# Performance work log

Hardware: AMD Instinct MI355X
Metric: run time of the kernel (lower is better)

The kernel has to match this reference:

```python
import jax, jax.numpy as jnp
import numpy as np

N = 50000      # nodes
E = 800000     # edges (avg degree 16)
F_IN = 128     # input_dim
HID = 64       # hidden_dim
HEADS = 4      # heads on first layer only
G = 512        # number of graphs in batch
EPS = 1e-5
NEG_SLOPE = 0.2

# (in_dim, out_dim, heads) per GATv2 layer
LAYER_DIMS = [(F_IN, HID, HEADS), (HID * HEADS, HID, 1), (HID, HID, 1)]


def setup_inputs() -> dict:
    key = jax.random.key(0)
    ks = jax.random.split(key, 16)
    def rn(k, shape, fan_in):
        return jax.random.normal(k, shape, jnp.float32) / np.float32(np.sqrt(fan_in))
    inp = {}
    inp["x"] = jax.random.normal(ks[0], (N, F_IN), jnp.float32)
    inp["edge_index"] = jax.random.randint(ks[1], (2, E), 0, N)
    inp["batch"] = jnp.sort(jax.random.randint(ks[2], (N,), 0, G))
    i = 3
    for l, (din, dout, h) in enumerate(LAYER_DIMS):
        kk = jax.random.split(ks[i], 3)
        inp[f"Wl{l}"] = rn(kk[0], (din, h * dout), din)
        inp[f"bl{l}"] = jnp.zeros((h * dout,), jnp.float32)
        inp[f"Wr{l}"] = rn(kk[1], (din, h * dout), din)
        inp[f"br{l}"] = jnp.zeros((h * dout,), jnp.float32)
        inp[f"att{l}"] = rn(kk[2], (h, dout), dout)
        inp[f"bias{l}"] = jnp.zeros((h * dout,), jnp.float32)
        inp[f"ln_g{l}"] = jnp.ones((h * dout,), jnp.float32)
        inp[f"ln_b{l}"] = jnp.zeros((h * dout,), jnp.float32)
        i += 1
    inp["Wh1"] = rn(ks[i], (HID, HID), HID)
    inp["bh1"] = jnp.zeros((HID,), jnp.float32)
    inp["Wh2"] = rn(ks[i + 1], (HID, 1), HID)
    inp["bh2"] = jnp.zeros((1,), jnp.float32)
    return inp


def gatv2_layer(x, src, dst, Wl, bl, Wr, br, att, bias, heads, out_c):
    """PyG GATv2Conv (concat=True, share_weights=False, eval mode)."""
    n = x.shape[0]
    xl = (x @ Wl + bl).reshape(n, heads, out_c)   # messages (source side)
    xr = (x @ Wr + br).reshape(n, heads, out_c)   # destination side
    e = jax.nn.leaky_relu(xl[src] + xr[dst], NEG_SLOPE)          # [E,H,C]
    logit = jnp.einsum('ehc,hc->eh', e, att)                      # [E,H]
    m = jax.ops.segment_max(logit, dst, num_segments=n)           # segment-softmax
    ex = jnp.exp(logit - m[dst])
    den = jax.ops.segment_sum(ex, dst, num_segments=n)
    alpha = ex / den[dst]                                         # [E,H]
    out = jax.ops.segment_sum(alpha[:, :, None] * xl[src], dst, num_segments=n)
    return out.reshape(n, heads * out_c) + bias


def graph_layernorm(h, g, b):
    """PyG LayerNorm(mode='graph') with batch=None: normalize over all elements."""
    mu = h.mean()
    xc = h - mu
    var = (xc * xc).mean()
    return xc * jax.lax.rsqrt(var + EPS) * g + b


def reference(x, edge_index, batch,
              Wl0, bl0, Wr0, br0, att0, bias0, ln_g0, ln_b0,
              Wl1, bl1, Wr1, br1, att1, bias1, ln_g1, ln_b1,
              Wl2, bl2, Wr2, br2, att2, bias2, ln_g2, ln_b2,
              Wh1, bh1, Wh2, bh2):
    src, dst = edge_index[0], edge_index[1]
    layers = [
        (Wl0, bl0, Wr0, br0, att0, bias0, ln_g0, ln_b0),
        (Wl1, bl1, Wr1, br1, att1, bias1, ln_g1, ln_b1),
        (Wl2, bl2, Wr2, br2, att2, bias2, ln_g2, ln_b2),
    ]
    h = x
    for (Wl, bl, Wr, br, att, bias, g, b), (_, dout, heads) in zip(layers, LAYER_DIMS):
        h_in = h
        h = gatv2_layer(h, src, dst, Wl, bl, Wr, br, att, bias, heads, dout)
        h = graph_layernorm(h, g, b)
        h = jax.nn.relu(h)
        if h_in.shape[1] == h.shape[1]:   # residual only when widths match
            h = h + h_in
        # dropout: identity in eval mode
    # global mean pool over graphs
    counts = jax.ops.segment_sum(jnp.ones((h.shape[0], 1), h.dtype), batch, num_segments=G)
    Z = jax.ops.segment_sum(h, batch, num_segments=G) / jnp.maximum(counts, 1.0)
    logits = jax.nn.relu(Z @ Wh1 + bh1) @ Wh2 + bh2
    return logits
```

## Files before the change

kernel.cpp:

```cpp
#include <hip/hip_runtime.h>
#include <math.h>

#define NN 50000
#define NE 800000
#define NG 512
#define LRELU 0.2f
#define LN_EPS 1e-5
#define GCAP 128
#define NBUCK 256

typedef __attribute__((ext_vector_type(8))) short short8;
typedef __attribute__((ext_vector_type(4))) float f32x4;

__global__ void hist_kernel(const int* __restrict__ dst, int* __restrict__ deg) {
    int e = blockIdx.x * blockDim.x + threadIdx.x;
    if (e < NE) atomicAdd(&deg[dst[e]], 1);
}

__global__ __launch_bounds__(1024) void scan1(const int* __restrict__ deg,
                                              int* __restrict__ excl,
                                              int* __restrict__ bsum, int n) {
    __shared__ int s[1024];
    int tid = threadIdx.x;
    int gid = blockIdx.x * 1024 + tid;
    int v = (gid < n) ? deg[gid] : 0;
    s[tid] = v;
    __syncthreads();
    for (int off = 1; off < 1024; off <<= 1) {
        int t = (tid >= off) ? s[tid - off] : 0;
        __syncthreads();
        s[tid] += t;
        __syncthreads();
    }
    if (gid < n) excl[gid] = s[tid] - v;
    if (tid == 1023) bsum[blockIdx.x] = s[1023];
}

__global__ __launch_bounds__(64) void scan2(int* __restrict__ bsum, int nb) {
    int lane = threadIdx.x;
    int v = (lane < nb) ? bsum[lane] : 0;
    int orig = v;
    #pragma unroll
    for (int off = 1; off < 64; off <<= 1) {
        int t = __shfl_up(v, off, 64);
        if (lane >= off) v += t;
    }
    if (lane < nb) bsum[lane] = v - orig;
}

__global__ __launch_bounds__(1024) void scan3(int* __restrict__ row_ptr,
                                              int* __restrict__ cursor,
                                              const int* __restrict__ bsum, int n) {
    int tid = threadIdx.x;
    int gid = blockIdx.x * 1024 + tid;
    if (gid < n) {
        int v = row_ptr[gid] + bsum[blockIdx.x];
        row_ptr[gid] = v;
        cursor[gid] = v;
    }
    if (gid == 0) row_ptr[n] = NE;
}

__global__ void scatter_kernel(const int* __restrict__ src, const int* __restrict__ dst,
                               int* __restrict__ cursor, int* __restrict__ col_src) {
    int e = blockIdx.x * blockDim.x + threadIdx.x;
    if (e < NE) {
        int pos = atomicAdd(&cursor[dst[e]], 1);
        col_src[pos] = src[e];
    }
}

__device__ inline void split_bf16(float v, ushort& h, ushort& l) {
    unsigned ub = __float_as_uint(v);
    unsigned hh = (ub + 0x7FFFu + ((ub >> 16) & 1u)) >> 16;
    float vh = __uint_as_float(hh << 16);
    float r = v - vh;
    unsigned ur = __float_as_uint(r);
    unsigned ll = (ur + 0x7FFFu + ((ur >> 16) & 1u)) >> 16;
    h = (ushort)hh; l = (ushort)ll;
}

__global__ __launch_bounds__(256) void prep_w(const float* __restrict__ Wl0,
                                              const float* __restrict__ Wr0,
                                              const float* __restrict__ Wl1,
                                              const float* __restrict__ Wr1,
                                              const float* __restrict__ Wl2,
                                              const float* __restrict__ Wr2,
                                              ushort* __restrict__ wt) {
    int id = blockIdx.x * 256 + threadIdx.x;
    const float* W; int K, N, rel; ushort* hi;
    if (id < 65536) {
        W = (id < 32768) ? Wl0 : Wr0;
        rel = id & 32767; K = 128; N = 256;
        hi = wt + ((id < 32768) ? 0 : 65536);
    } else if (id < 98304) {
        int t = id - 65536;
        W = (t < 16384) ? Wl1 : Wr1;
        rel = t & 16383; K = 256; N = 64;
        hi = wt + 131072 + ((t < 16384) ? 0 : 32768);
    } else if (id < 106496) {
        int t = id - 98304;
        W = (t < 4096) ? Wl2 : Wr2;
        rel = t & 4095; K = 64; N = 64;
        hi = wt + 196608 + ((t < 4096) ? 0 : 8192);
    } else return;
    ushort* lo = hi + K * N;
    int n = rel / K, k = rel - n * K;
    ushort h, l;
    split_bf16(W[k * N + n], h, l);
    hi[rel] = h;
    lo[rel] = l;
}

__global__ __launch_bounds__(256) void gemm_mfma(const float* __restrict__ A,
                                                 const ushort* __restrict__ Bh0,
                                                 const ushort* __restrict__ Bl0,
                                                 const float* __restrict__ bias0,
                                                 float* __restrict__ C0,
                                                 const ushort* __restrict__ Bh1,
                                                 const ushort* __restrict__ Bl1,
                                                 const float* __restrict__ bias1,
                                                 float* __restrict__ C1,
                                                 int M, int Ncol, int K,
                                                 const float* __restrict__ lnstats,
                                                 const float* __restrict__ lng,
                                                 const float* __restrict__ lnb) {
    __shared__ ushort sAh[64][40];
    __shared__ ushort sAl[64][40];
    __shared__ ushort sBh[64][40];
    __shared__ ushort sBl[64][40];
    const ushort* Bhi = blockIdx.z ? Bh1 : Bh0;
    const ushort* Blo = blockIdx.z ? Bl1 : Bl0;
    const float*  bias = blockIdx.z ? bias1 : bias0;
    float*        C = blockIdx.z ? C1 : C0;
    const int tid = threadIdx.x;
    const int row0 = blockIdx.x * 64;
    const int col0 = blockIdx.y * 64;
    const int w = tid >> 6, lane = tid & 63;
    const int fm = lane & 15;
    const int fk = (lane >> 4) * 8;
    const bool doln = (lnstats != nullptr);
    float mu = 0.f, rstd = 0.f;
    if (doln) { mu = lnstats[0]; rstd = lnstats[1]; }
    f32x4 acc[4] = {};

    for (int k0 = 0; k0 < K; k0 += 32) {
        __syncthreads();
        int f = tid;
        #pragma unroll
        for (int it = 0; it < 2; it++, f += 256) {
            int r = f >> 3, kc = (f & 7) * 4;
            int grow = row0 + r;
            float4 v = (grow < M) ? *(const float4*)&A[(size_t)grow * K + k0 + kc]
                                  : make_float4(0.f, 0.f, 0.f, 0.f);
            if (doln) {
                int c0 = k0 + kc;
                v.x = fmaxf((v.x - mu) * rstd * lng[c0 + 0] + lnb[c0 + 0], 0.f);
                v.y = fmaxf((v.y - mu) * rstd * lng[c0 + 1] + lnb[c0 + 1], 0.f);
                v.z = fmaxf((v.z - mu) * rstd * lng[c0 + 2] + lnb[c0 + 2], 0.f);
                v.w = fmaxf((v.w - mu) * rstd * lng[c0 + 3] + lnb[c0 + 3], 0.f);
            }
            ushort4 h, l;
            split_bf16(v.x, h.x, l.x);
            split_bf16(v.y, h.y, l.y);
            split_bf16(v.z, h.z, l.z);
            split_bf16(v.w, h.w, l.w);
            *(ushort4*)&sAh[r][kc] = h;
            *(ushort4*)&sAl[r][kc] = l;
        }
        int u = tid;
        #pragma unroll
        for (int it = 0; it < 2; it++, u += 256) {
            int n = u >> 3, kc = (u & 7) * 4;
            *(ushort4*)&sBh[n][kc] = *(const ushort4*)&Bhi[(size_t)(col0 + n) * K + k0 + kc];
            *(ushort4*)&sBl[n][kc] = *(const ushort4*)&Blo[(size_t)(col0 + n) * K + k0 + kc];
        }
        __syncthreads();
        short8 ah = *(const short8*)&sAh[w * 16 + fm][fk];
        short8 al = *(const short8*)&sAl[w * 16 + fm][fk];
        #pragma unroll
        for (int c = 0; c < 4; c++) {
            short8 bh = *(const short8*)&sBh[c * 16 + fm][fk];
            short8 bl = *(const short8*)&sBl[c * 16 + fm][fk];
            acc[c] = __builtin_amdgcn_mfma_f32_16x16x32_bf16(ah, bh, acc[c], 0, 0, 0);
            acc[c] = __builtin_amdgcn_mfma_f32_16x16x32_bf16(al, bh, acc[c], 0, 0, 0);
            acc[c] = __builtin_amdgcn_mfma_f32_16x16x32_bf16(ah, bl, acc[c], 0, 0, 0);
        }
    }
    const int orow = w * 16 + (lane >> 4) * 4;
    #pragma unroll
    for (int c = 0; c < 4; c++) {
        int col = col0 + c * 16 + fm;
        float bv = bias[col];
        #pragma unroll
        for (int r = 0; r < 4; r++) {
            int grow = row0 + orow + r;
            if (grow < M) C[(size_t)grow * Ncol + col] = acc[c][r] + bv;
        }
    }
}

__device__ inline float dpp_red_add16(float x) {
    x += __int_as_float(__builtin_amdgcn_update_dpp(0, __float_as_int(x), 0xB1, 0xF, 0xF, true));
    x += __int_as_float(__builtin_amdgcn_update_dpp(0, __float_as_int(x), 0x4E, 0xF, 0xF, true));
    x += __int_as_float(__builtin_amdgcn_update_dpp(0, __float_as_int(x), 0x141, 0xF, 0xF, true));
    x += __int_as_float(__builtin_amdgcn_update_dpp(0, __float_as_int(x), 0x140, 0xF, 0xF, true));
    return x;
}

__device__ inline void gat_upd_fast(const float4& xv, const float4& rxr, const float4& ratt,
                                    float& m, float& sum, float4& acc) {
    float vx = xv.x + rxr.x; vx = fmaxf(vx, vx * LRELU);
    float vy = xv.y + rxr.y; vy = fmaxf(vy, vy * LRELU);
    float vz = xv.z + rxr.z; vz = fmaxf(vz, vz * LRELU);
    float vw = xv.w + rxr.w; vw = fmaxf(vw, vw * LRELU);
    float p = vx * ratt.x;
    p = fmaf(vy, ratt.y, p);
    p = fmaf(vz, ratt.z, p);
    p = fmaf(vw, ratt.w, p);
    p = dpp_red_add16(p);
    if (__all(p <= m)) {
        float e = __expf(p - m);
        sum += e;
        acc.x = fmaf(e, xv.x, acc.x);
        acc.y = fmaf(e, xv.y, acc.y);
        acc.z = fmaf(e, xv.z, acc.z);
        acc.w = fmaf(e, xv.w, acc.w);
    } else {
        float mn = fmaxf(m, p);
        float sc = __expf(m - mn);
        float e  = __expf(p - mn);
        sum = fmaf(sum, sc, e);
        acc.x = fmaf(acc.x, sc, e * xv.x);
        acc.y = fmaf(acc.y, sc, e * xv.y);
        acc.z = fmaf(acc.z, sc, e * xv.z);
        acc.w = fmaf(acc.w, sc, e * xv.w);
        m = mn;
    }
}

__global__ __launch_bounds__(256) void gat4(const float* __restrict__ xl,
                                            const float* __restrict__ xr,
                                            const float* __restrict__ att,
                                            const float* __restrict__ bias,
                                            const int* __restrict__ row_ptr,
                                            const int* __restrict__ col_src,
                                            float* __restrict__ out,
                                            double* __restrict__ red) {
    __shared__ int scol[4][GCAP];
    __shared__ double bs1[4], bs2[4];
    const int tid = threadIdx.x;
    const int w = tid >> 6, lane = tid & 63;
    const int n = blockIdx.x * 4 + w;
    const int base = row_ptr[n];
    int deg = row_ptr[n + 1] - base;
    if (deg > GCAP) deg = GCAP;
    for (int j = lane; j < deg; j += 64) scol[w][j] = col_src[base + j];
    const float4 rxr  = ((const float4*)(xr + (size_t)n * 256))[lane];
    const float4 ratt = ((const float4*)att)[lane];
    __syncthreads();

    float m = -1e30f, sum = 0.f;
    float4 acc = {0.f, 0.f, 0.f, 0.f};
    if (deg > 0) {
        const int dm1 = deg - 1;
        float4 xv0 = ((const float4*)(xl + (size_t)scol[w][0] * 256))[lane];
        float4 xv1 = ((const float4*)(xl + (size_t)scol[w][(1 < dm1) ? 1 : dm1] * 256))[lane];
        for (int j = 0; j < deg; j++) {
            float4 xv = xv0;
            xv0 = xv1;
            int idx = (j + 2 < deg) ? j + 2 : dm1;
            xv1 = ((const float4*)(xl + (size_t)scol[w][idx] * 256))[lane];
            gat_upd_fast(xv, rxr, ratt, m, sum, acc);
        }
    }
    float rden = (sum > 0.f) ? 1.f / sum : 0.f;
    float4 bv = ((const float4*)bias)[lane];
    float4 o;
    o.x = fmaf(acc.x, rden, bv.x);
    o.y = fmaf(acc.y, rden, bv.y);
    o.z = fmaf(acc.z, rden, bv.z);
    o.w = fmaf(acc.w, rden, bv.w);
    ((float4*)(out + (size_t)n * 256))[lane] = o;

    float z1 = o.x + o.y + o.z + o.w;
    float z2 = o.x * o.x + o.y * o.y + o.z * o.z + o.w * o.w;
    #pragma unroll
    for (int off = 32; off > 0; off >>= 1) {
        z1 += __shfl_xor(z1, off, 64);
        z2 += __shfl_xor(z2, off, 64);
    }
    if (lane == 0) { bs1[w] = (double)z1; bs2[w] = (double)z2; }
    __syncthreads();
    if (tid == 0) {
        double t1 = bs1[0] + bs1[1] + bs1[2] + bs1[3];
        double t2 = bs2[0] + bs2[1] + bs2[2] + bs2[3];
        int b = (blockIdx.x & (NBUCK - 1)) * 2;
        atomicAdd(&red[b], t1);
        atomicAdd(&red[b + 1], t2);
    }
}

__global__ __launch_bounds__(256) void gat1(const float* __restrict__ xl,
                                            const float* __restrict__ xr,
                                            const float* __restrict__ att,
                                            const float* __restrict__ bias,
                                            const int* __restrict__ row_ptr,
                                            const int* __restrict__ col_src,
                                            float* __restrict__ out,
                                            double* __restrict__ red) {
    __shared__ int scol[4][GCAP];
    __shared__ double bs1[4], bs2[4];
    const int tid = threadIdx.x;
    const int w = tid >> 6, lane = tid & 63;
    const int n = blockIdx.x * 4 + w;
    const int g = lane >> 4, li = lane & 15;
    const int base = row_ptr[n];
    int deg = row_ptr[n + 1] - base;
    if (deg > GCAP) deg = GCAP;
    for (int j = lane; j < deg; j += 64) scol[w][j] = col_src[base + j];
    const float4 rxr  = ((const float4*)(xr + (size_t)n * 64))[li];
    const float4 ratt = ((const float4*)att)[li];
    __syncthreads();

    float m = -1e30f, sum = 0.f;
    float4 acc = {0.f, 0.f, 0.f, 0.f};
    if (deg > 0) {
        const int dm1 = deg - 1;
        auto Lg = [&](int j) {
            int idx = (j < dm1) ? j : dm1;
            return ((const float4*)(xl + (size_t)scol[w][idx] * 64))[li];
        };
        float4 xv0 = Lg(g), xv1 = Lg(g + 4);
        for (int j = g; j < deg; j += 4) {
            float4 xv = xv0;
            xv0 = xv1;
            xv1 = Lg(j + 8);
            gat_upd_fast(xv, rxr, ratt, m, sum, acc);
        }
    }
    #pragma unroll
    for (int off = 16; off < 64; off <<= 1) {
        float m2 = __shfl_xor(m, off, 64);
        float z2 = __shfl_xor(sum, off, 64);
        float ax = __shfl_xor(acc.x, off, 64);
        float ay = __shfl_xor(acc.y, off, 64);
        float az = __shfl_xor(acc.z, off, 64);
        float aw = __shfl_xor(acc.w, off, 64);
        float M = fmaxf(m, m2);
        float e1 = __expf(m - M), e2 = __expf(m2 - M);
        sum   = sum   * e1 + z2 * e2;
        acc.x = acc.x * e1 + ax * e2;
        acc.y = acc.y * e1 + ay * e2;
        acc.z = acc.z * e1 + az * e2;
        acc.w = acc.w * e1 + aw * e2;
        m = M;
    }
    float rden = (sum > 0.f) ? 1.f / sum : 0.f;
    float4 bv = ((const float4*)bias)[li];
    float4 o;
    o.x = fmaf(acc.x, rden, bv.x);
    o.y = fmaf(acc.y, rden, bv.y);
    o.z = fmaf(acc.z, rden, bv.z);
    o.w = fmaf(acc.w, rden, bv.w);
    if (g == 0) ((float4*)(out + (size_t)n * 64))[li] = o;

    float z1 = (g == 0) ? (o.x + o.y + o.z + o.w) : 0.f;
    float z2 = (g == 0) ? (o.x * o.x + o.y * o.y + o.z * o.z + o.w * o.w) : 0.f;
    #pragma unroll
    for (int off = 32; off > 0; off >>= 1) {
        z1 += __shfl_xor(z1, off, 64);
        z2 += __shfl_xor(z2, off, 64);
    }
    if (lane == 0) { bs1[w] = (double)z1; bs2[w] = (double)z2; }
    __syncthreads();
    if (tid == 0) {
        double t1 = bs1[0] + bs1[1] + bs1[2] + bs1[3];
        double t2 = bs2[0] + bs2[1] + bs2[2] + bs2[3];
        int b = (blockIdx.x & (NBUCK - 1)) * 2;
        atomicAdd(&red[b], t1);
        atomicAdd(&red[b + 1], t2);
    }
}

__global__ __launch_bounds__(NBUCK) void finalize_stats(const double* __restrict__ red,
                                                        float* __restrict__ stats, int M) {
    __shared__ double sa[NBUCK], sb[NBUCK];
    int t = threadIdx.x;
    sa[t] = red[t * 2];
    sb[t] = red[t * 2 + 1];
    __syncthreads();
    for (int off = NBUCK / 2; off > 0; off >>= 1) {
        if (t < off) { sa[t] += sa[t + off]; sb[t] += sb[t + off]; }
        __syncthreads();
    }
    if (t == 0) {
        double mu = sa[0] / M;
        double var = sb[0] / M - mu * mu;
        stats[0] = (float)mu;
        stats[1] = (float)(1.0 / sqrt(var + LN_EPS));
    }
}

#define PLB 256
__global__ __launch_bounds__(256) void pool_ln(const float* __restrict__ C2,
                                               const float* __restrict__ D,
                                               const float* __restrict__ stats,
                                               const float* __restrict__ g1,
                                               const float* __restrict__ b1,
                                               const float* __restrict__ g2,
                                               const float* __restrict__ b2,
                                               const int* __restrict__ batch,
                                               float* __restrict__ Zsum,
                                               int* __restrict__ gcount) {
    const int wid = blockIdx.x * 4 + (threadIdx.x >> 6);
    const int lane = threadIdx.x & 63;
    const int NW = PLB * 4;
    const int per = (NN + NW - 1) / NW;
    int n0 = wid * per;
    int n1 = n0 + per; if (n1 > NN) n1 = NN;
    if (n0 >= n1) return;
    const float mu1 = stats[2], r1 = stats[3], mu2 = stats[4], r2 = stats[5];
    const float ga = r1 * g1[lane], ba = fmaf(-mu1, ga, b1[lane]);
    const float gb = r2 * g2[lane], bb = fmaf(-mu2, gb, b2[lane]);
    float zacc = 0.f; int cnt = 0; int cur = batch[n0];
    for (int n = n0; n < n1; n++) {
        int gi = batch[n];
        if (gi != cur) {
            atomicAdd(&Zsum[cur * 64 + lane], zacc);
            if (lane == 0) atomicAdd(&gcount[cur], cnt);
            zacc = 0.f; cnt = 0; cur = gi;
        }
        float hin = fmaxf(fmaf(D[(size_t)n * 64 + lane], ga, ba), 0.f);
        float v = fmaxf(fmaf(C2[(size_t)n * 64 + lane], gb, bb), 0.f) + hin;
        zacc += v; cnt++;
    }
    atomicAdd(&Zsum[cur * 64 + lane], zacc);
    if (lane == 0) atomicAdd(&gcount[cur], cnt);
}

__global__ __launch_bounds__(64) void mlp_head(const float* __restrict__ Zsum,
                                               const int* __restrict__ gcount,
                                               const float* __restrict__ Wh1,
                                               const float* __restrict__ bh1,
                                               const float* __restrict__ Wh2,
                                               const float* __restrict__ bh2,
                                               float* __restrict__ out) {
    __shared__ float sz[64];
    int g = blockIdx.x, tid = threadIdx.x;
    int cnt = gcount[g];
    float inv = 1.f / (float)(cnt > 1 ? cnt : 1);
    sz[tid] = Zsum[g * 64 + tid] * inv;
    __syncthreads();
    float acc = bh1[tid];
    #pragma unroll
    for (int c = 0; c < 64; c++) acc = fmaf(sz[c], Wh1[c * 64 + tid], acc);
    acc = fmaxf(acc, 0.f);
    float v = acc * Wh2[tid];
    #pragma unroll
    for (int off = 32; off > 0; off >>= 1) v += __shfl_xor(v, off, 64);
    if (tid == 0) out[g] = v + bh2[0];
}

extern "C" void kernel_launch(void* const* d_in, const int* in_sizes, int n_in,
                              void* d_out, int out_size, void* d_ws, size_t ws_size,
                              hipStream_t stream) {
    (void)in_sizes; (void)n_in; (void)out_size; (void)ws_size;
    const float* x     = (const float*)d_in[0];
    const int*   ei    = (const int*)d_in[1];
    const int*   batch = (const int*)d_in[2];
    const float* Wl0 = (const float*)d_in[3];  const float* bl0 = (const float*)d_in[4];
    const float* Wr0 = (const float*)d_in[5];  const float* br0 = (const float*)d_in[6];
    const float* at0 = (const float*)d_in[7];  const float* bi0 = (const float*)d_in[8];
    const float* lg0 = (const float*)d_in[9];  const float* lb0 = (const float*)d_in[10];
    const float* Wl1 = (const float*)d_in[11]; const float* bl1 = (const float*)d_in[12];
    const float* Wr1 = (const float*)d_in[13]; const float* br1 = (const float*)d_in[14];
    const float* at1 = (const float*)d_in[15]; const float* bi1 = (const float*)d_in[16];
    const float* lg1 = (const float*)d_in[17]; const float* lb1 = (const float*)d_in[18];
    const float* Wl2 = (const float*)d_in[19]; const float* bl2 = (const float*)d_in[20];
    const float* Wr2 = (const float*)d_in[21]; const float* br2 = (const float*)d_in[22];
    const float* at2 = (const float*)d_in[23]; const float* bi2 = (const float*)d_in[24];
    const float* lg2 = (const float*)d_in[25]; const float* lb2 = (const float*)d_in[26];
    const float* Wh1 = (const float*)d_in[27]; const float* bh1 = (const float*)d_in[28];
    const float* Wh2 = (const float*)d_in[29]; const float* bh2 = (const float*)d_in[30];
    float* out = (float*)d_out;

    const int* srcp = ei;
    const int* dstp = ei + NE;

    char* w = (char*)d_ws;
    size_t off = 0;
    auto carve = [&](size_t bytes) -> void* {
        void* p = w + off;
        off += (bytes + 255) & ~(size_t)255;
        return p;
    };
    float* A = (float*)carve((size_t)NN * 256 * 4);
    float* B = (float*)carve((size_t)NN * 256 * 4);
    float* C = (float*)carve((size_t)NN * 256 * 4);
    float* D = (float*)carve((size_t)NN * 64 * 4);
    ushort* wt = (ushort*)carve(212992 * 2);
    const size_t REDB = (size_t)3 * NBUCK * 2 * sizeof(double);
    size_t zbytes = REDB + (size_t)NG * 64 * 4 + NG * 4 + (size_t)NN * 4;
    char* zb = (char*)carve(zbytes);
    double* red   = (double*)zb;
    float*  Zsum  = (float*)(zb + REDB);
    int*    gcnt  = (int*)(zb + REDB + (size_t)NG * 64 * 4);
    int*    deg   = (int*)(zb + REDB + (size_t)NG * 64 * 4 + NG * 4);
    int* row_ptr = (int*)carve((size_t)(NN + 1) * 4);
    int* cursor  = (int*)carve((size_t)NN * 4);
    int* col_src = (int*)carve((size_t)NE * 4);
    int* bsum    = (int*)carve(64 * 4);
    float* stats = (float*)carve(6 * 4);

    const ushort* W0lh = wt;           const ushort* W0ll = wt + 32768;
    const ushort* W0rh = wt + 65536;   const ushort* W0rl = wt + 98304;
    const ushort* W1lh = wt + 131072;  const ushort* W1ll = wt + 147456;
    const ushort* W1rh = wt + 163840;  const ushort* W1rl = wt + 180224;
    const ushort* W2lh = wt + 196608;  const ushort* W2ll = wt + 200704;
    const ushort* W2rh = wt + 204800;  const ushort* W2rl = wt + 208896;

    hipMemsetAsync(zb, 0, zbytes, stream);
    prep_w<<<416, 256, 0, stream>>>(Wl0, Wr0, Wl1, Wr1, Wl2, Wr2, wt);

    hist_kernel<<<(NE + 255) / 256, 256, 0, stream>>>(dstp, deg);
    const int SB = (NN + 1023) / 1024;
    scan1<<<SB, 1024, 0, stream>>>(deg, row_ptr, bsum, NN);
    scan2<<<1, 64, 0, stream>>>(bsum, SB);
    scan3<<<SB, 1024, 0, stream>>>(row_ptr, cursor, bsum, NN);
    scatter_kernel<<<(NE + 255) / 256, 256, 0, stream>>>(srcp, dstp, cursor, col_src);

    const int GR = (NN + 63) / 64;
    const int GATB = NN / 4;

    gemm_mfma<<<dim3(GR, 4, 2), 256, 0, stream>>>(x, W0lh, W0ll, bl0, A,
                                                  W0rh, W0rl, br0, B, NN, 256, 128,
                                                  nullptr, nullptr, nullptr);
    gat4<<<GATB, 256, 0, stream>>>(A, B, at0, bi0, row_ptr, col_src, C, red);
    finalize_stats<<<1, NBUCK, 0, stream>>>(red, stats, NN * 256);

    gemm_mfma<<<dim3(GR, 1, 2), 256, 0, stream>>>(C, W1lh, W1ll, bl1, A,
                                                  W1rh, W1rl, br1, B, NN, 64, 256,
                                                  stats, lg0, lb0);
    gat1<<<GATB, 256, 0, stream>>>(A, B, at1, bi1, row_ptr, col_src, D, red + 2 * NBUCK);
    finalize_stats<<<1, NBUCK, 0, stream>>>(red + 2 * NBUCK, stats + 2, NN * 64);

    gemm_mfma<<<dim3(GR, 1, 2), 256, 0, stream>>>(D, W2lh, W2ll, bl2, A,
                                                  W2rh, W2rl, br2, B, NN, 64, 64,
                                                  stats + 2, lg1, lb1);
    gat1<<<GATB, 256, 0, stream>>>(A, B, at2, bi2, row_ptr, col_src, C, red + 4 * NBUCK);
    finalize_stats<<<1, NBUCK, 0, stream>>>(red + 4 * NBUCK, stats + 4, NN * 64);

    pool_ln<<<PLB, 256, 0, stream>>>(C, D, stats, lg1, lb1, lg2, lb2,
                                     batch, Zsum, gcnt);
    mlp_head<<<NG, 64, 0, stream>>>(Zsum, gcnt, Wh1, bh1, Wh2, bh2, out);
}
```

Baseline: 553.7 us.

## Fuse scan/stat finalize kernels into consumers, widen layer-0 GEMM, deepen gather prefetch

Removes the scan2 and three finalize_stats launches by recomputing the block-prefix base inside scan3 and the LayerNorm statistics inside each consuming GEMM and pool kernel. The layer-0 GEMM block now computes all 256 output columns, so each A tile is loaded and split into bf16 once instead of four times. The GAT gather loops get a deeper software prefetch (4 buffers in gat4, 2 per group in gat1) with padded index buffers so the clamp on the index is no longer needed. The trade-offs are redundant stat reductions in every block, larger LDS and register use in the wide GEMM, and more loads in flight per wave.

New measurement: 572.5 us. 3.4% more time.

```diff
diff --git a/kernel.cpp b/kernel.cpp
--- a/kernel.cpp
+++ b/kernel.cpp
@@ -36,25 +36,21 @@
     if (tid == 1023) bsum[blockIdx.x] = s[1023];
 }
 
-__global__ __launch_bounds__(64) void scan2(int* __restrict__ bsum, int nb) {
-    int lane = threadIdx.x;
-    int v = (lane < nb) ? bsum[lane] : 0;
-    int orig = v;
-    #pragma unroll
-    for (int off = 1; off < 64; off <<= 1) {
-        int t = __shfl_up(v, off, 64);
-        if (lane >= off) v += t;
-    }
-    if (lane < nb) bsum[lane] = v - orig;
-}
-
 __global__ __launch_bounds__(1024) void scan3(int* __restrict__ row_ptr,
                                               int* __restrict__ cursor,
                                               const int* __restrict__ bsum, int n) {
+    __shared__ int sbase;
     int tid = threadIdx.x;
+    if (tid < 64) {
+        int v = (tid < (int)blockIdx.x) ? bsum[tid] : 0;
+        #pragma unroll
+        for (int off = 32; off > 0; off >>= 1) v += __shfl_xor(v, off, 64);
+        if (tid == 0) sbase = v;
+    }
+    __syncthreads();
     int gid = blockIdx.x * 1024 + tid;
     if (gid < n) {
-        int v = row_ptr[gid] + bsum[blockIdx.x];
+        int v = row_ptr[gid] + sbase;
         row_ptr[gid] = v;
         cursor[gid] = v;
     }
@@ -112,6 +108,7 @@
     lo[rel] = l;
 }
 
+template<int NCB, bool DOLN>
 __global__ __launch_bounds__(256) void gemm_mfma(const float* __restrict__ A,
                                                  const ushort* __restrict__ Bh0,
                                                  const ushort* __restrict__ Bl0,
@@ -122,27 +119,45 @@
                                                  const float* __restrict__ bias1,
                                                  float* __restrict__ C1,
                                                  int M, int Ncol, int K,
-                                                 const float* __restrict__ lnstats,
+                                                 const double* __restrict__ red,
+                                                 int Mdiv,
                                                  const float* __restrict__ lng,
                                                  const float* __restrict__ lnb) {
     __shared__ ushort sAh[64][40];
     __shared__ ushort sAl[64][40];
-    __shared__ ushort sBh[64][40];
-    __shared__ ushort sBl[64][40];
-    const ushort* Bhi = blockIdx.z ? Bh1 : Bh0;
-    const ushort* Blo = blockIdx.z ? Bl1 : Bl0;
-    const float*  bias = blockIdx.z ? bias1 : bias0;
-    float*        C = blockIdx.z ? C1 : C0;
+    __shared__ ushort sBh[64 * NCB][40];
+    __shared__ ushort sBl[64 * NCB][40];
+    __shared__ float sstat[2];
+    const ushort* Bhi = blockIdx.y ? Bh1 : Bh0;
+    const ushort* Blo = blockIdx.y ? Bl1 : Bl0;
+    const float*  bias = blockIdx.y ? bias1 : bias0;
+    float*        C = blockIdx.y ? C1 : C0;
     const int tid = threadIdx.x;
     const int row0 = blockIdx.x * 64;
-    const int col0 = blockIdx.y * 64;
     const int w = tid >> 6, lane = tid & 63;
     const int fm = lane & 15;
     const int fk = (lane >> 4) * 8;
-    const bool doln = (lnstats != nullptr);
     float mu = 0.f, rstd = 0.f;
-    if (doln) { mu = lnstats[0]; rstd = lnstats[1]; }
-    f32x4 acc[4] = {};
+    if constexpr (DOLN) {
+        if (tid < 64) {
+            double sa = 0, sb = 0;
+            for (int i = lane; i < NBUCK; i += 64) { sa += red[2 * i]; sb += red[2 * i + 1]; }
+            #pragma unroll
+            for (int off = 32; off > 0; off >>= 1) {
+                sa += __shfl_xor(sa, off, 64);
+                sb += __shfl_xor(sb, off, 64);
+            }
+            if (lane == 0) {
+                double m_ = sa / Mdiv;
+                double v_ = sb / Mdiv - m_ * m_;
+                sstat[0] = (float)m_;
+                sstat[1] = (float)(1.0 / sqrt(v_ + LN_EPS));
+            }
+        }
+        __syncthreads();
+        mu = sstat[0]; rstd = sstat[1];
+    }
+    f32x4 acc[4 * NCB] = {};
 
     for (int k0 = 0; k0 < K; k0 += 32) {
         __syncthreads();
@@ -153,7 +168,7 @@
             int grow = row0 + r;
             float4 v = (grow < M) ? *(const float4*)&A[(size_t)grow * K + k0 + kc]
                                   : make_float4(0.f, 0.f, 0.f, 0.f);
-            if (doln) {
+            if constexpr (DOLN) {
                 int c0 = k0 + kc;
                 v.x = fmaxf((v.x - mu) * rstd * lng[c0 + 0] + lnb[c0 + 0], 0.f);
                 v.y = fmaxf((v.y - mu) * rstd * lng[c0 + 1] + lnb[c0 + 1], 0.f);
@@ -170,16 +185,16 @@
         }
         int u = tid;
         #pragma unroll
-        for (int it = 0; it < 2; it++, u += 256) {
+        for (int it = 0; it < 2 * NCB; it++, u += 256) {
             int n = u >> 3, kc = (u & 7) * 4;
-            *(ushort4*)&sBh[n][kc] = *(const ushort4*)&Bhi[(size_t)(col0 + n) * K + k0 + kc];
-            *(ushort4*)&sBl[n][kc] = *(const ushort4*)&Blo[(size_t)(col0 + n) * K + k0 + kc];
+            *(ushort4*)&sBh[n][kc] = *(const ushort4*)&Bhi[(size_t)n * K + k0 + kc];
+            *(ushort4*)&sBl[n][kc] = *(const ushort4*)&Blo[(size_t)n * K + k0 + kc];
         }
         __syncthreads();
         short8 ah = *(const short8*)&sAh[w * 16 + fm][fk];
         short8 al = *(const short8*)&sAl[w * 16 + fm][fk];
         #pragma unroll
-        for (int c = 0; c < 4; c++) {
+        for (int c = 0; c < 4 * NCB; c++) {
             short8 bh = *(const short8*)&sBh[c * 16 + fm][fk];
             short8 bl = *(const short8*)&sBl[c * 16 + fm][fk];
             acc[c] = __builtin_amdgcn_mfma_f32_16x16x32_bf16(ah, bh, acc[c], 0, 0, 0);
@@ -189,8 +204,8 @@
     }
     const int orow = w * 16 + (lane >> 4) * 4;
     #pragma unroll
-    for (int c = 0; c < 4; c++) {
-        int col = col0 + c * 16 + fm;
+    for (int c = 0; c < 4 * NCB; c++) {
+        int col = c * 16 + fm;
         float bv = bias[col];
         #pragma unroll
         for (int r = 0; r < 4; r++) {
@@ -247,7 +262,7 @@
                                             const int* __restrict__ col_src,
                                             float* __restrict__ out,
                                             double* __restrict__ red) {
-    __shared__ int scol[4][GCAP];
+    __shared__ int scol[4][GCAP + 8];
     __shared__ double bs1[4], bs2[4];
     const int tid = threadIdx.x;
     const int w = tid >> 6, lane = tid & 63;
@@ -256,6 +271,7 @@
     int deg = row_ptr[n + 1] - base;
     if (deg > GCAP) deg = GCAP;
     for (int j = lane; j < deg; j += 64) scol[w][j] = col_src[base + j];
+    if (deg > 0 && lane < 8) scol[w][deg + lane] = col_src[base + deg - 1];
     const float4 rxr  = ((const float4*)(xr + (size_t)n * 256))[lane];
     const float4 ratt = ((const float4*)att)[lane];
     __syncthreads();
@@ -263,16 +279,21 @@
     float m = -1e30f, sum = 0.f;
     float4 acc = {0.f, 0.f, 0.f, 0.f};
     if (deg > 0) {
-        const int dm1 = deg - 1;
-        float4 xv0 = ((const float4*)(xl + (size_t)scol[w][0] * 256))[lane];
-        float4 xv1 = ((const float4*)(xl + (size_t)scol[w][(1 < dm1) ? 1 : dm1] * 256))[lane];
-        for (int j = 0; j < deg; j++) {
-            float4 xv = xv0;
-            xv0 = xv1;
-            int idx = (j + 2 < deg) ? j + 2 : dm1;
-            xv1 = ((const float4*)(xl + (size_t)scol[w][idx] * 256))[lane];
-            gat_upd_fast(xv, rxr, ratt, m, sum, acc);
-        }
+        auto LD = [&](int j) {
+            return ((const float4*)(xl + (size_t)scol[w][j] * 256))[lane];
+        };
+        float4 b0 = LD(0), b1 = LD(1), b2 = LD(2), b3 = LD(3);
+        int j = 0;
+        for (; j + 4 <= deg; j += 4) {
+            gat_upd_fast(b0, rxr, ratt, m, sum, acc); b0 = LD(j + 4);
+            gat_upd_fast(b1, rxr, ratt, m, sum, acc); b1 = LD(j + 5);
+            gat_upd_fast(b2, rxr, ratt, m, sum, acc); b2 = LD(j + 6);
+            gat_upd_fast(b3, rxr, ratt, m, sum, acc); b3 = LD(j + 7);
+        }
+        int r = deg - j;
+        if (r > 0) gat_upd_fast(b0, rxr, ratt, m, sum, acc);
+        if (r > 1) gat_upd_fast(b1, rxr, ratt, m, sum, acc);
+        if (r > 2) gat_upd_fast(b2, rxr, ratt, m, sum, acc);
     }
     float rden = (sum > 0.f) ? 1.f / sum : 0.f;
     float4 bv = ((const float4*)bias)[lane];
@@ -309,7 +330,7 @@
                                             const int* __restrict__ col_src,
                                             float* __restrict__ out,
                                             double* __restrict__ red) {
-    __shared__ int scol[4][GCAP];
+    __shared__ int scol[4][GCAP + 16];
     __shared__ double bs1[4], bs2[4];
     const int tid = threadIdx.x;
     const int w = tid >> 6, lane = tid & 63;
@@ -319,6 +340,7 @@
     int deg = row_ptr[n + 1] - base;
     if (deg > GCAP) deg = GCAP;
     for (int j = lane; j < deg; j += 64) scol[w][j] = col_src[base + j];
+    if (deg > 0 && lane < 16) scol[w][deg + lane] = col_src[base + deg - 1];
     const float4 rxr  = ((const float4*)(xr + (size_t)n * 64))[li];
     const float4 ratt = ((const float4*)att)[li];
     __syncthreads();
@@ -326,17 +348,13 @@
     float m = -1e30f, sum = 0.f;
     float4 acc = {0.f, 0.f, 0.f, 0.f};
     if (deg > 0) {
-        const int dm1 = deg - 1;
-        auto Lg = [&](int j) {
-            int idx = (j < dm1) ? j : dm1;
-            return ((const float4*)(xl + (size_t)scol[w][idx] * 64))[li];
+        auto LD = [&](int j) {
+            return ((const float4*)(xl + (size_t)scol[w][j] * 64))[li];
         };
-        float4 xv0 = Lg(g), xv1 = Lg(g + 4);
-        for (int j = g; j < deg; j += 4) {
-            float4 xv = xv0;
-            xv0 = xv1;
-            xv1 = Lg(j + 8);
-            gat_upd_fast(xv, rxr, ratt, m, sum, acc);
+        float4 a = LD(g), b = LD(g + 4);
+        for (int j = g; j < deg; j += 8) {
+            gat_upd_fast(a, rxr, ratt, m, sum, acc); a = LD(j + 8);
+            if (j + 4 < deg) { gat_upd_fast(b, rxr, ratt, m, sum, acc); b = LD(j + 12); }
         }
     }
     #pragma unroll
@@ -383,29 +401,10 @@
     }
 }
 
-__global__ __launch_bounds__(NBUCK) void finalize_stats(const double* __restrict__ red,
-                                                        float* __restrict__ stats, int M) {
-    __shared__ double sa[NBUCK], sb[NBUCK];
-    int t = threadIdx.x;
-    sa[t] = red[t * 2];
-    sb[t] = red[t * 2 + 1];
-    __syncthreads();
-    for (int off = NBUCK / 2; off > 0; off >>= 1) {
-        if (t < off) { sa[t] += sa[t + off]; sb[t] += sb[t + off]; }
-        __syncthreads();
-    }
-    if (t == 0) {
-        double mu = sa[0] / M;
-        double var = sb[0] / M - mu * mu;
-        stats[0] = (float)mu;
-        stats[1] = (float)(1.0 / sqrt(var + LN_EPS));
-    }
-}
-
 #define PLB 256
 __global__ __launch_bounds__(256) void pool_ln(const float* __restrict__ C2,
                                                const float* __restrict__ D,
-                                               const float* __restrict__ stats,
+                                               const double* __restrict__ red,
                                                const float* __restrict__ g1,
                                                const float* __restrict__ b1,
                                                const float* __restrict__ g2,
@@ -413,14 +412,33 @@
                                                const int* __restrict__ batch,
                                                float* __restrict__ Zsum,
                                                int* __restrict__ gcount) {
-    const int wid = blockIdx.x * 4 + (threadIdx.x >> 6);
+    __shared__ float sst[4];
+    const int w = threadIdx.x >> 6;
     const int lane = threadIdx.x & 63;
+    if (w < 2) {
+        const double* rp = red + (w + 1) * 2 * NBUCK;
+        double sa = 0, sb = 0;
+        for (int i = lane; i < NBUCK; i += 64) { sa += rp[2 * i]; sb += rp[2 * i + 1]; }
+        #pragma unroll
+        for (int off = 32; off > 0; off >>= 1) {
+            sa += __shfl_xor(sa, off, 64);
+            sb += __shfl_xor(sb, off, 64);
+        }
+        if (lane == 0) {
+            double m_ = sa / (double)(NN * 64);
+            double v_ = sb / (double)(NN * 64) - m_ * m_;
+            sst[w * 2]     = (float)m_;
+            sst[w * 2 + 1] = (float)(1.0 / sqrt(v_ + LN_EPS));
+        }
+    }
+    __syncthreads();
+    const float mu1 = sst[0], r1 = sst[1], mu2 = sst[2], r2 = sst[3];
+    const int wid = blockIdx.x * 4 + w;
     const int NW = PLB * 4;
     const int per = (NN + NW - 1) / NW;
     int n0 = wid * per;
     int n1 = n0 + per; if (n1 > NN) n1 = NN;
     if (n0 >= n1) return;
-    const float mu1 = stats[2], r1 = stats[3], mu2 = stats[4], r2 = stats[5];
     const float ga = r1 * g1[lane], ba = fmaf(-mu1, ga, b1[lane]);
     const float gb = r2 * g2[lane], bb = fmaf(-mu2, gb, b2[lane]);
     float zacc = 0.f; int cnt = 0; int cur = batch[n0];
@@ -511,7 +529,6 @@
     int* cursor  = (int*)carve((size_t)NN * 4);
     int* col_src = (int*)carve((size_t)NE * 4);
     int* bsum    = (int*)carve(64 * 4);
-    float* stats = (float*)carve(6 * 4);
 
     const ushort* W0lh = wt;           const ushort* W0ll = wt + 32768;
     const ushort* W0rh = wt + 65536;   const ushort* W0rl = wt + 98304;
@@ -526,32 +543,28 @@
     hist_kernel<<<(NE + 255) / 256, 256, 0, stream>>>(dstp, deg);
     const int SB = (NN + 1023) / 1024;
     scan1<<<SB, 1024, 0, stream>>>(deg, row_ptr, bsum, NN);
-    scan2<<<1, 64, 0, stream>>>(bsum, SB);
     scan3<<<SB, 1024, 0, stream>>>(row_ptr, cursor, bsum, NN);
     scatter_kernel<<<(NE + 255) / 256, 256, 0, stream>>>(srcp, dstp, cursor, col_src);
 
     const int GR = (NN + 63) / 64;
     const int GATB = NN / 4;
 
-    gemm_mfma<<<dim3(GR, 4, 2), 256, 0, stream>>>(x, W0lh, W0ll, bl0, A,
-                                                  W0rh, W0rl, br0, B, NN, 256, 128,
-                                                  nullptr, nullptr, nullptr);
+    gemm_mfma<4, false><<<dim3(GR, 2), 256, 0, stream>>>(x, W0lh, W0ll, bl0, A,
+                                                         W0rh, W0rl, br0, B, NN, 256, 128,
+                                                         nullptr, 1, nullptr, nullptr);
     gat4<<<GATB, 256, 0, stream>>>(A, B, at0, bi0, row_ptr, col_src, C, red);
-    finalize_stats<<<1, NBUCK, 0, stream>>>(red, stats, NN * 256);
-
-    gemm_mfma<<<dim3(GR, 1, 2), 256, 0, stream>>>(C, W1lh, W1ll, bl1, A,
-                                                  W1rh, W1rl, br1, B, NN, 64, 256,
-                                                  stats, lg0, lb0);
+
+    gemm_mfma<1, true><<<dim3(GR, 2), 256, 0, stream>>>(C, W1lh, W1ll, bl1, A,
+                                                        W1rh, W1rl, br1, B, NN, 64, 256,
+                                                        red, NN * 256, lg0, lb0);
     gat1<<<GATB, 256, 0, stream>>>(A, B, at1, bi1, row_ptr, col_src, D, red + 2 * NBUCK);
-    finalize_stats<<<1, NBUCK, 0, stream>>>(red + 2 * NBUCK, stats + 2, NN * 64);
-
-    gemm_mfma<<<dim3(GR, 1, 2), 256, 0, stream>>>(D, W2lh, W2ll, bl2, A,
-                                                  W2rh, W2rl, br2, B, NN, 64, 64,
-                                                  stats + 2, lg1, lb1);
+
+    gemm_mfma<1, true><<<dim3(GR, 2), 256, 0, stream>>>(D, W2lh, W2ll, bl2, A,
+                                                        W2rh, W2rl, br2, B, NN, 64, 64,
+                                                        red + 2 * NBUCK, NN * 64, lg1, lb1);
     gat1<<<GATB, 256, 0, stream>>>(A, B, at2, bi2, row_ptr, col_src, C, red + 4 * NBUCK);
-    finalize_stats<<<1, NBUCK, 0, stream>>>(red + 4 * NBUCK, stats + 4, NN * 64);
-
-    pool_ln<<<PLB, 256, 0, stream>>>(C, D, stats, lg1, lb1, lg2, lb2,
+
+    pool_ln<<<PLB, 256, 0, stream>>>(C, D, red, lg1, lb1, lg2, lb2,
                                      batch, Zsum, gcnt);
     mlp_head<<<NG, 64, 0, stream>>>(Zsum, gcnt, Wh1, bh1, Wh2, bh2, out);
 }
```
